# Optimization experiments

Measured on AMD Instinct MI355X. Metric: run time of the kernel, lower is better.

## Reference

```python
import jax, jax.numpy as jnp
import numpy as np


def setup_inputs() -> dict:
    key = jax.random.key(0)
    ks = jax.random.split(key, 15)
    B, r, d, h, na = 64, 64, 2048, 64, 256
    x = jax.random.normal(ks[0], (B, d, na), dtype=jnp.float32)
    L = jax.random.randint(ks[1], (B, 2, na), 0, 2).astype(jnp.float32)
    p = lambda i, shp: jax.random.normal(ks[i], shp, dtype=jnp.float32)
    return {
        "x": x, "L": L,
        "Aq": p(2, (r, d)), "Ak": p(3, (r, d)), "Av": p(4, (r, d)),
        "Aq1": p(5, (r, r)), "Ak1": p(6, (r, r)), "Av1": p(7, (r, r)),
        "Aq5": p(8, (r, r)), "Ak5": p(9, (r, r)), "Av5": p(10, (r, r)),
        "Ao": p(11, (r, r)), "Ao1": p(12, (r, r)), "Ao5": p(13, (h, r)),
    }


def reference(x, L, Aq, Ak, Av, Aq1, Ak1, Av1, Aq5, Ak5, Av5, Ao, Ao1, Ao5):
    B, d, na = x.shape
    # numNeighbors: count of L[:,0,:] >= 1 per batch, +1 -> [B,1,1]
    numN = jnp.sum((L[:, 0, :] >= 1.0).astype(jnp.float32), axis=1)[:, None, None] + 1.0
    scale = jnp.sqrt(numN)  # [B,1,1]

    def attn(M, Wq, Wk, Wv):
        # M: [B, f, na]; Wq/Wk/Wv: [r, f]
        Q = jax.nn.sigmoid(jnp.einsum('rf,bfn->bnr', Wq, M))  # [B,na,r]
        K = jax.nn.sigmoid(jnp.einsum('rf,bfn->brn', Wk, M))  # [B,r,na]
        V = jax.nn.sigmoid(jnp.einsum('rf,bfn->bnr', Wv, M))  # [B,na,r]
        A = jax.nn.softmax(jnp.einsum('bnr,brm->bnm', Q, K) / scale, axis=2)
        return jnp.einsum('bnm,bmr->brn', A, V)  # [B,r,na]

    o = attn(x, Aq, Ak, Av)
    M = jax.nn.silu(jnp.einsum('sr,brn->bsn', Ao, o))
    o = attn(M, Aq1, Ak1, Av1)
    M = jax.nn.silu(jnp.einsum('sr,brn->bsn', Ao1, o))
    o = attn(M, Aq5, Ak5, Av5)
    M = jax.nn.silu(jnp.einsum('hr,brn->bhn', Ao5, o))  # [B,h,na]

    blk = d // na  # rows per block (8)
    def diagvec(i):
        # kron(sum-of-squares, ones(1,2)) == repeat each element twice -> [B, 2*na]
        return jnp.repeat(jnp.sum(M[:, i * blk:(i + 1) * blk, :] ** 2, axis=1), 2, axis=1)

    M11, M12, M21, M22 = diagvec(0), diagvec(1), diagvec(2), diagvec(3)
    Mpp = jnp.sum(M[:, 4 * blk:, :] ** 2, axis=1)  # [B, na]

    # q = x[:, :4, :].transpose(1,2).reshape(B, 4*na) (agent-major ordering)
    q = jnp.transpose(x[:, :4, :], (0, 2, 1)).reshape(B, 4 * na)
    q1, q2 = q[:, :2 * na], q[:, 2 * na:]
    # Block matrix [[diag(M11), diag(M12)], [diag(M21), diag(M22)]] quadratic form,
    # computed without materializing the [B, 4na, 4na] matrix.
    quad = jnp.sum(M11 * q1 * q1 + M12 * q1 * q2 + M21 * q2 * q1 + M22 * q2 * q2,
                   axis=1, keepdims=True)
    return quad + jnp.sum(Mpp, axis=1, keepdims=True)  # [B, 1]
```

## Files before the change

### kernel.cpp

```cpp
#include <hip/hip_runtime.h>
#include <stdint.h>

typedef _Float16 f16;
typedef f16 f16x8 __attribute__((ext_vector_type(8)));
typedef float f32x4 __attribute__((ext_vector_type(4)));

#define MFMA(a,b,c) __builtin_amdgcn_mfma_f32_16x16x32_f16(a, b, c, 0, 0, 0)

__device__ __forceinline__ float sigmoidf_(float z) {
  return __builtin_amdgcn_rcpf(1.0f + __expf(-z));
}

__global__ void prep_kernel(const float* __restrict__ L,
    const float* __restrict__ Aq, const float* __restrict__ Ak, const float* __restrict__ Av,
    const float* __restrict__ Aq1, const float* __restrict__ Ak1, const float* __restrict__ Av1,
    const float* __restrict__ Aq5, const float* __restrict__ Ak5, const float* __restrict__ Av5,
    const float* __restrict__ Ao, const float* __restrict__ Ao1, const float* __restrict__ Ao5,
    float* __restrict__ scale, f16* __restrict__ Wcat, f16* __restrict__ Wsm,
    float* __restrict__ out)
{
  __shared__ float r4[4];
  int blk = blockIdx.x, t = threadIdx.x;
  if (blk < 64) {
    float v = (L[blk * 512 + t] >= 1.0f) ? 1.0f : 0.0f;
    #pragma unroll
    for (int off = 32; off; off >>= 1) v += __shfl_down(v, off);
    if ((t & 63) == 0) r4[t >> 6] = v;
    __syncthreads();
    if (t == 0) scale[blk] = sqrtf(r4[0] + r4[1] + r4[2] + r4[3] + 1.0f);
  } else if (blk < 160) {
    int base = (blk - 64) * 4096;
    for (int i = 0; i < 16; i++) {
      int idx = base + t + i * 256;
      int row = idx >> 11, col = idx & 2047;
      float v = (row < 64) ? Aq[row * 2048 + col]
              : (row < 128) ? Ak[(row - 64) * 2048 + col]
              : Av[(row - 128) * 2048 + col];
      Wcat[idx] = (f16)v;
    }
  } else if (blk < 169) {
    int j = blk - 160;
    const float* s = (j == 0) ? Aq1 : (j == 1) ? Ak1 : (j == 2) ? Av1 : (j == 3) ? Aq5
                   : (j == 4) ? Ak5 : (j == 5) ? Av5 : (j == 6) ? Ao : (j == 7) ? Ao1 : Ao5;
    for (int i = 0; i < 16; i++) { int idx = t + i * 256; Wsm[j * 4096 + idx] = (f16)s[idx]; }
  } else {
    if (t < 64) out[t] = 0.0f;
  }
}

__global__ __launch_bounds__(256) void qkv1_kernel(const float* __restrict__ x,
    const f16* __restrict__ Wcat, f16* __restrict__ Qt, f16* __restrict__ Kt,
    f16* __restrict__ Vg)
{
  int b = blockIdx.y, n0 = blockIdx.x * 32;
  int t = threadIdx.x, lane = t & 63, w = t >> 6;
  int l15 = lane & 15, q = lane >> 4;
  __shared__ f16 xt[2][32 * 72];
  __shared__ f16 wt[2][192 * 72];
  f32x4 acc[2][3] = {};
  const float* xb = x + (size_t)b * 524288 + n0;
  int tn = t & 31, fg = t >> 5;

  int r0 = t >> 3,           c0 = t & 7;
  int r1 = (t + 256) >> 3,   c1 = (t + 256) & 7;
  int r2 = (t + 512) >> 3,   c2 = (t + 512) & 7;
  int r3 = (t + 768) >> 3,   c3 = (t + 768) & 7;
  int r4 = (t + 1024) >> 3,  c4 = (t + 1024) & 7;
  int r5 = (t + 1280) >> 3,  c5 = (t + 1280) & 7;
  const f16* pw0 = Wcat + (size_t)r0 * 2048 + c0 * 8;
  const f16* pw1 = Wcat + (size_t)r1 * 2048 + c1 * 8;
  const f16* pw2 = Wcat + (size_t)r2 * 2048 + c2 * 8;
  const f16* pw3 = Wcat + (size_t)r3 * 2048 + c3 * 8;
  const f16* pw4 = Wcat + (size_t)r4 * 2048 + c4 * 8;
  const f16* pw5 = Wcat + (size_t)r5 * 2048 + c5 * 8;
  const float* px = xb + (size_t)(fg * 8) * 256 + tn;

  float xa0, xa1, xa2, xa3, xa4, xa5, xa6, xa7;
  uint4 wr0, wr1, wr2, wr3, wr4, wr5;

#define LOAD_X(f0n) do {                                                        \
    const float* xp_ = px + (size_t)(f0n) * 256;                                \
    xa0 = xp_[0];    xa1 = xp_[256];  xa2 = xp_[512];  xa3 = xp_[768];          \
    xa4 = xp_[1024]; xa5 = xp_[1280]; xa6 = xp_[1536]; xa7 = xp_[1792];         \
  } while (0)

#define LOAD_W(f0n) do {                                                        \
    wr0 = *(const uint4*)(pw0 + (f0n)); wr1 = *(const uint4*)(pw1 + (f0n));     \
    wr2 = *(const uint4*)(pw2 + (f0n)); wr3 = *(const uint4*)(pw3 + (f0n));     \
    wr4 = *(const uint4*)(pw4 + (f0n)); wr5 = *(const uint4*)(pw5 + (f0n));     \
  } while (0)

#define WRITE_XW(buf) do {                                                      \
    f16x8 pk_;                                                                  \
    pk_[0] = (f16)xa0; pk_[1] = (f16)xa1; pk_[2] = (f16)xa2; pk_[3] = (f16)xa3; \
    pk_[4] = (f16)xa4; pk_[5] = (f16)xa5; pk_[6] = (f16)xa6; pk_[7] = (f16)xa7; \
    *(f16x8*)&xt[buf][tn * 72 + fg * 8] = pk_;                                  \
    f16* wb_ = &wt[buf][0];                                                     \
    *(uint4*)&wb_[r0 * 72 + c0 * 8] = wr0;                                      \
    *(uint4*)&wb_[r1 * 72 + c1 * 8] = wr1;                                      \
    *(uint4*)&wb_[r2 * 72 + c2 * 8] = wr2;                                      \
    *(uint4*)&wb_[r3 * 72 + c3 * 8] = wr3;                                      \
    *(uint4*)&wb_[r4 * 72 + c4 * 8] = wr4;                                      \
    *(uint4*)&wb_[r5 * 72 + c5 * 8] = wr5;                                      \
  } while (0)

  LOAD_X(0);
  LOAD_W(0);
  WRITE_XW(0);
  __syncthreads();

  int cur = 0;
  for (int f0 = 0; f0 < 2048; f0 += 64) {
    int nxt = cur ^ 1;
    bool more = (f0 + 64 < 2048);
    if (more) { LOAD_X(f0 + 64); LOAD_W(f0 + 64); }

    #pragma unroll
    for (int ks = 0; ks < 2; ks++) {
      int k0 = ks * 32 + q * 8;
      f16x8 af[2], bf[3];
      af[0] = *(const f16x8*)&xt[cur][l15 * 72 + k0];
      af[1] = *(const f16x8*)&xt[cur][(16 + l15) * 72 + k0];
      #pragma unroll
      for (int j = 0; j < 3; j++) bf[j] = *(const f16x8*)&wt[cur][((w * 3 + j) * 16 + l15) * 72 + k0];
      #pragma unroll
      for (int nt = 0; nt < 2; nt++)
        #pragma unroll
        for (int j = 0; j < 3; j++)
          acc[nt][j] = MFMA(af[nt], bf[j], acc[nt][j]);
    }

    if (more) WRITE_XW(nxt);
    __syncthreads();
    cur = nxt;
  }
#undef LOAD_X
#undef LOAD_W
#undef WRITE_XW

  #pragma unroll
  for (int nt = 0; nt < 2; nt++)
    #pragma unroll
    for (int j = 0; j < 3; j++) {
      int rr = (w * 3 + j) * 16 + l15;
      float s[4];
      #pragma unroll
      for (int reg = 0; reg < 4; reg++) s[reg] = sigmoidf_(acc[nt][j][reg]);
      int nbase = n0 + nt * 16 + q * 4;
      if (rr < 64) {
        #pragma unroll
        for (int reg = 0; reg < 4; reg++)
          Qt[(size_t)b * 16384 + (size_t)(nbase + reg) * 64 + rr] = (f16)s[reg];
      } else if (rr < 128) {
        #pragma unroll
        for (int reg = 0; reg < 4; reg++)
          Kt[(size_t)b * 16384 + (size_t)(nbase + reg) * 64 + (rr - 64)] = (f16)s[reg];
      } else {
        union { f16 h[4]; uint2 u; } pk;
        #pragma unroll
        for (int reg = 0; reg < 4; reg++) pk.h[reg] = (f16)s[reg];
        *(uint2*)(Vg + (size_t)b * 16384 + (size_t)(rr - 128) * 256 + nbase) = pk.u;
      }
    }
}

template<int LAYER>
__global__ __launch_bounds__(512) void attnB_kernel(const float* __restrict__ x,
    const float* __restrict__ scale, const f16* __restrict__ Wsm,
    const f16* __restrict__ Qtg, const f16* __restrict__ Ktg, const f16* __restrict__ Vgg,
    const f16* __restrict__ Min, f16* __restrict__ Mout, float* __restrict__ out)
{
  int g = blockIdx.x, b = blockIdx.y, n0 = g * 64;
  int t = threadIdx.x, lane = t & 63, w = t >> 6;
  int l15 = lane & 15, q = lane >> 4;
  __shared__ f16 KT[256 * 72];
  __shared__ f16 SM[256 * 72];
  __shared__ f16 VM[64 * 264];
  __shared__ f16 QT[64 * 72];
  __shared__ f16 OT[64 * 72];
  __shared__ float denomS[64];

  float sinv = __builtin_amdgcn_rcpf(scale[b]);
  if (t < 64) denomS[t] = 0.0f;

  if (LAYER == 0) {
    const uint4* qs = (const uint4*)(Qtg + (size_t)b * 16384 + (size_t)n0 * 64);
    { int n = t >> 3, c = t & 7; *(uint4*)&QT[n * 72 + c * 8] = qs[t]; }
    const uint4* ks = (const uint4*)(Ktg + (size_t)b * 16384);
    const uint4* vs = (const uint4*)(Vgg + (size_t)b * 16384);
    #pragma unroll
    for (int i = 0; i < 4; i++) {
      int id = t + i * 512;
      int m = id >> 3, c = id & 7;
      *(uint4*)&KT[m * 72 + c * 8] = ks[id];
      int r = id >> 5, c2 = id & 31;
      *(uint4*)&VM[r * 264 + c2 * 8] = vs[id];
    }
  } else {
    const uint4* ms = (const uint4*)(Min + (size_t)b * 16384);
    #pragma unroll
    for (int i = 0; i < 4; i++) {
      int id = t + i * 512, m = id >> 3, c = id & 7;
      *(uint4*)&SM[m * 72 + c * 8] = ms[id];
    }
  }
  __syncthreads();

  const f16* Wq = Wsm + (size_t)(LAYER == 1 ? 0 : 3) * 4096;
  const f16* Wk = Wsm + (size_t)(LAYER == 1 ? 1 : 4) * 4096;
  const f16* Wv = Wsm + (size_t)(LAYER == 1 ? 2 : 5) * 4096;
  const f16* Wo = Wsm + (size_t)(LAYER == 0 ? 6 : (LAYER == 1 ? 7 : 8)) * 4096;

  if (LAYER > 0) {
    if (w < 4) {
      f16x8 bk[4][2];
      #pragma unroll
      for (int rt = 0; rt < 4; rt++) {
        bk[rt][0] = *(const f16x8*)(Wk + (rt * 16 + l15) * 64 + q * 8);
        bk[rt][1] = *(const f16x8*)(Wk + (rt * 16 + l15) * 64 + 32 + q * 8);
      }
      #pragma unroll
      for (int mi = 0; mi < 4; mi++) {
        int mt = w * 4 + mi;
        f16x8 a0 = *(const f16x8*)&SM[(mt * 16 + l15) * 72 + q * 8];
        f16x8 a1 = *(const f16x8*)&SM[(mt * 16 + l15) * 72 + 32 + q * 8];
        #pragma unroll
        for (int rt = 0; rt < 4; rt++) {
          f32x4 acc = {}; acc = MFMA(a0, bk[rt][0], acc); acc = MFMA(a1, bk[rt][1], acc);
          #pragma unroll
          for (int reg = 0; reg < 4; reg++)
            KT[(mt * 16 + q * 4 + reg) * 72 + rt * 16 + l15] = (f16)sigmoidf_(acc[reg]);
        }
      }
    } else {
      f16x8 av[4][2];
      #pragma unroll
      for (int rt = 0; rt < 4; rt++) {
        av[rt][0] = *(const f16x8*)(Wv + (rt * 16 + l15) * 64 + q * 8);
        av[rt][1] = *(const f16x8*)(Wv + (rt * 16 + l15) * 64 + 32 + q * 8);
      }
      #pragma unroll
      for (int mi = 0; mi < 4; mi++) {
        int mt = (w - 4) * 4 + mi;
        f16x8 b0 = *(const f16x8*)&SM[(mt * 16 + l15) * 72 + q * 8];
        f16x8 b1 = *(const f16x8*)&SM[(mt * 16 + l15) * 72 + 32 + q * 8];
        #pragma unroll
        for (int rt = 0; rt < 4; rt++) {
          f32x4 acc = {}; acc = MFMA(av[rt][0], b0, acc); acc = MFMA(av[rt][1], b1, acc);
          #pragma unroll
          for (int reg = 0; reg < 4; reg++)
            VM[(rt * 16 + q * 4 + reg) * 264 + mt * 16 + l15] = (f16)sigmoidf_(acc[reg]);
        }
      }
    }
    {
      int nt = w >> 1;
      f16x8 a0 = *(const f16x8*)&SM[(n0 + nt * 16 + l15) * 72 + q * 8];
      f16x8 a1 = *(const f16x8*)&SM[(n0 + nt * 16 + l15) * 72 + 32 + q * 8];
      #pragma unroll
      for (int j = 0; j < 2; j++) {
        int rt = (w & 1) * 2 + j;
        f16x8 b0 = *(const f16x8*)(Wq + (rt * 16 + l15) * 64 + q * 8);
        f16x8 b1 = *(const f16x8*)(Wq + (rt * 16 + l15) * 64 + 32 + q * 8);
        f32x4 acc = {}; acc = MFMA(a0, b0, acc); acc = MFMA(a1, b1, acc);
        #pragma unroll
        for (int reg = 0; reg < 4; reg++)
          QT[(nt * 16 + q * 4 + reg) * 72 + rt * 16 + l15] = (f16)sigmoidf_(acc[reg]);
      }
    }
    __syncthreads();
  }

  {
    int nt = w >> 1;
    f16x8 a0 = *(const f16x8*)&QT[(nt * 16 + l15) * 72 + q * 8];
    f16x8 a1 = *(const f16x8*)&QT[(nt * 16 + l15) * 72 + 32 + q * 8];
    float dsum[4] = {0.f, 0.f, 0.f, 0.f};
    #pragma unroll
    for (int mi = 0; mi < 8; mi++) {
      int mt = (w & 1) * 8 + mi;
      f16x8 b0 = *(const f16x8*)&KT[(mt * 16 + l15) * 72 + q * 8];
      f16x8 b1 = *(const f16x8*)&KT[(mt * 16 + l15) * 72 + 32 + q * 8];
      f32x4 acc = {}; acc = MFMA(a0, b0, acc); acc = MFMA(a1, b1, acc);
      #pragma unroll
      for (int reg = 0; reg < 4; reg++) {
        float e = __expf(acc[reg] * sinv);
        dsum[reg] += e;
        SM[(nt * 16 + q * 4 + reg) * 264 + mt * 16 + l15] = (f16)e;
      }
    }
    #pragma unroll
    for (int reg = 0; reg < 4; reg++) {
      #pragma unroll
      for (int mask = 1; mask < 16; mask <<= 1) dsum[reg] += __shfl_xor(dsum[reg], mask);
    }
    if (l15 == 0) {
      #pragma unroll
      for (int reg = 0; reg < 4; reg++) atomicAdd(&denomS[nt * 16 + q * 4 + reg], dsum[reg]);
    }
  }
  __syncthreads();

  {
    int nt = w >> 1;
    f32x4 oacc[2] = {};
    #pragma unroll
    for (int kc = 0; kc < 8; kc++) {
      f16x8 af = *(const f16x8*)&SM[(nt * 16 + l15) * 264 + kc * 32 + q * 8];
      #pragma unroll
      for (int j = 0; j < 2; j++) {
        int rt = (w & 1) * 2 + j;
        f16x8 bf = *(const f16x8*)&VM[(rt * 16 + l15) * 264 + kc * 32 + q * 8];
        oacc[j] = MFMA(af, bf, oacc[j]);
      }
    }
    float rden[4];
    #pragma unroll
    for (int reg = 0; reg < 4; reg++)
      rden[reg] = __builtin_amdgcn_rcpf(denomS[nt * 16 + q * 4 + reg]);
    #pragma unroll
    for (int j = 0; j < 2; j++) {
      int rt = (w & 1) * 2 + j;
      #pragma unroll
      for (int reg = 0; reg < 4; reg++) {
        int row = nt * 16 + q * 4 + reg;
        OT[row * 72 + rt * 16 + l15] = (f16)(oacc[j][reg] * rden[reg]);
      }
    }
  }
  __syncthreads();

  f16* Mst = QT;
  {
    int nt = w >> 1;
    f16x8 a0 = *(const f16x8*)&OT[(nt * 16 + l15) * 72 + q * 8];
    f16x8 a1 = *(const f16x8*)&OT[(nt * 16 + l15) * 72 + 32 + q * 8];
    #pragma unroll
    for (int j = 0; j < 2; j++) {
      int st = (w & 1) * 2 + j;
      f16x8 b0 = *(const f16x8*)(Wo + (st * 16 + l15) * 64 + q * 8);
      f16x8 b1 = *(const f16x8*)(Wo + (st * 16 + l15) * 64 + 32 + q * 8);
      f32x4 acc = {}; acc = MFMA(a0, b0, acc); acc = MFMA(a1, b1, acc);
      #pragma unroll
      for (int reg = 0; reg < 4; reg++) {
        float z = acc[reg];
        Mst[(nt * 16 + q * 4 + reg) * 64 + st * 16 + l15] = (f16)(z * sigmoidf_(z));
      }
    }
  }
  __syncthreads();

  if (LAYER < 2) {
    int row = t >> 3, c = t & 7;
    *(uint4*)(Mout + (size_t)b * 16384 + (size_t)(n0 + row) * 64 + c * 8)
        = *(const uint4*)&Mst[row * 64 + c * 8];
  } else {
    float contrib = 0.0f;
    if (t < 64) {
      int ntok = n0 + t;
      const f16* row = &Mst[t * 64];
      float d[4] = {0, 0, 0, 0}, pp = 0.0f;
      #pragma unroll
      for (int gg = 0; gg < 8; gg++) {
        f16x8 v = *(const f16x8*)(row + gg * 8);
        float ss = 0.0f;
        #pragma unroll
        for (int k = 0; k < 8; k++) { float f = (float)v[k]; ss += f * f; }
        if (gg < 4) d[gg] = ss; else pp += ss;
      }
      int np = ntok >> 1, c0 = (ntok & 1) * 2;
      const float* xb = x + (size_t)b * 524288 + (size_t)c0 * 256;
      float q1a = xb[np], q1b = xb[256 + np];
      float q2a = xb[128 + np], q2b = xb[384 + np];
      contrib = d[0] * (q1a * q1a + q1b * q1b)
              + (d[1] + d[2]) * (q1a * q2a + q1b * q2b)
              + d[3] * (q2a * q2a + q2b * q2b) + pp;
    }
    if (w == 0) {
      #pragma unroll
      for (int off = 32; off; off >>= 1) contrib += __shfl_down(contrib, off);
      if (lane == 0) atomicAdd(out + b, contrib);
    }
  }
}

extern "C" void kernel_launch(void* const* d_in, const int* in_sizes, int n_in,
                              void* d_out, int out_size, void* d_ws, size_t ws_size,
                              hipStream_t stream) {
  const float* x   = (const float*)d_in[0];
  const float* L   = (const float*)d_in[1];
  const float* Aq  = (const float*)d_in[2];
  const float* Ak  = (const float*)d_in[3];
  const float* Av  = (const float*)d_in[4];
  const float* Aq1 = (const float*)d_in[5];
  const float* Ak1 = (const float*)d_in[6];
  const float* Av1 = (const float*)d_in[7];
  const float* Aq5 = (const float*)d_in[8];
  const float* Ak5 = (const float*)d_in[9];
  const float* Av5 = (const float*)d_in[10];
  const float* Ao  = (const float*)d_in[11];
  const float* Ao1 = (const float*)d_in[12];
  const float* Ao5 = (const float*)d_in[13];

  char* ws = (char*)d_ws;
  float* scale = (float*)ws;
  f16* Wcat  = (f16*)(ws + 256);
  f16* Wsm   = (f16*)(ws + 786688);
  f16* Qtg   = (f16*)(ws + 860416);
  f16* Ktg   = (f16*)(ws + 2957568);
  f16* Vgg   = (f16*)(ws + 5054720);
  f16* MbufA = (f16*)(ws + 7151872);
  f16* MbufB = (f16*)(ws + 9249024);
  float* out = (float*)d_out;

  prep_kernel<<<170, 256, 0, stream>>>(L, Aq, Ak, Av, Aq1, Ak1, Av1,
                                       Aq5, Ak5, Av5, Ao, Ao1, Ao5, scale, Wcat, Wsm, out);
  qkv1_kernel<<<dim3(8, 64), 256, 0, stream>>>(x, Wcat, Qtg, Ktg, Vgg);
  attnB_kernel<0><<<dim3(4, 64), 512, 0, stream>>>(x, scale, Wsm, Qtg, Ktg, Vgg,
                                                   nullptr, MbufA, out);
  attnB_kernel<1><<<dim3(4, 64), 512, 0, stream>>>(x, scale, Wsm, Qtg, Ktg, Vgg,
                                                   MbufA, MbufB, out);
  attnB_kernel<2><<<dim3(4, 64), 512, 0, stream>>>(x, scale, Wsm, Qtg, Ktg, Vgg,
                                                   MbufB, nullptr, out);
}
```

Before: 265.4 us.

## Widen qkv1 token tile to 64 and double attention block threads

The QKV projection kernel now uses 512-thread blocks that each cover 64 tokens, so every weight tile staged in shared memory is reused across twice as many tokens and the weight traffic per token is halved. The attention kernels move to 1024 threads per block, giving each wave a smaller slice of the QK, PV and output-projection MFMA work. This is meant to raise parallelism and weight reuse. The cost is half as many qkv1 blocks (256 instead of 512) and heavier block-wide synchronisation, with more idle threads in the copy phases.

```diff
diff --git a/kernel.cpp b/kernel.cpp
--- a/kernel.cpp
+++ b/kernel.cpp
@@ -48,35 +48,30 @@
   }
 }
 
-__global__ __launch_bounds__(256) void qkv1_kernel(const float* __restrict__ x,
+__global__ __launch_bounds__(512, 4) void qkv1_kernel(const float* __restrict__ x,
     const f16* __restrict__ Wcat, f16* __restrict__ Qt, f16* __restrict__ Kt,
     f16* __restrict__ Vg)
 {
-  int b = blockIdx.y, n0 = blockIdx.x * 32;
+  int b = blockIdx.y, n0 = blockIdx.x * 64;
   int t = threadIdx.x, lane = t & 63, w = t >> 6;
   int l15 = lane & 15, q = lane >> 4;
-  __shared__ f16 xt[2][32 * 72];
+  __shared__ f16 xt[2][64 * 72];
   __shared__ f16 wt[2][192 * 72];
   f32x4 acc[2][3] = {};
   const float* xb = x + (size_t)b * 524288 + n0;
-  int tn = t & 31, fg = t >> 5;
+  int tn = t & 63, fg = t >> 6;
+  int nh = w >> 2, wr_ = w & 3;
 
   int r0 = t >> 3,           c0 = t & 7;
-  int r1 = (t + 256) >> 3,   c1 = (t + 256) & 7;
-  int r2 = (t + 512) >> 3,   c2 = (t + 512) & 7;
-  int r3 = (t + 768) >> 3,   c3 = (t + 768) & 7;
-  int r4 = (t + 1024) >> 3,  c4 = (t + 1024) & 7;
-  int r5 = (t + 1280) >> 3,  c5 = (t + 1280) & 7;
+  int r1 = (t + 512) >> 3,   c1 = (t + 512) & 7;
+  int r2 = (t + 1024) >> 3,  c2 = (t + 1024) & 7;
   const f16* pw0 = Wcat + (size_t)r0 * 2048 + c0 * 8;
   const f16* pw1 = Wcat + (size_t)r1 * 2048 + c1 * 8;
   const f16* pw2 = Wcat + (size_t)r2 * 2048 + c2 * 8;
-  const f16* pw3 = Wcat + (size_t)r3 * 2048 + c3 * 8;
-  const f16* pw4 = Wcat + (size_t)r4 * 2048 + c4 * 8;
-  const f16* pw5 = Wcat + (size_t)r5 * 2048 + c5 * 8;
   const float* px = xb + (size_t)(fg * 8) * 256 + tn;
 
   float xa0, xa1, xa2, xa3, xa4, xa5, xa6, xa7;
-  uint4 wr0, wr1, wr2, wr3, wr4, wr5;
+  uint4 wr0, wr1, wr2;
 
 #define LOAD_X(f0n) do {                                                        \
     const float* xp_ = px + (size_t)(f0n) * 256;                                \
@@ -86,8 +81,7 @@
 
 #define LOAD_W(f0n) do {                                                        \
     wr0 = *(const uint4*)(pw0 + (f0n)); wr1 = *(const uint4*)(pw1 + (f0n));     \
-    wr2 = *(const uint4*)(pw2 + (f0n)); wr3 = *(const uint4*)(pw3 + (f0n));     \
-    wr4 = *(const uint4*)(pw4 + (f0n)); wr5 = *(const uint4*)(pw5 + (f0n));     \
+    wr2 = *(const uint4*)(pw2 + (f0n));                                         \
   } while (0)
 
 #define WRITE_XW(buf) do {                                                      \
@@ -99,9 +93,6 @@
     *(uint4*)&wb_[r0 * 72 + c0 * 8] = wr0;                                      \
     *(uint4*)&wb_[r1 * 72 + c1 * 8] = wr1;                                      \
     *(uint4*)&wb_[r2 * 72 + c2 * 8] = wr2;                                      \
-    *(uint4*)&wb_[r3 * 72 + c3 * 8] = wr3;                                      \
-    *(uint4*)&wb_[r4 * 72 + c4 * 8] = wr4;                                      \
-    *(uint4*)&wb_[r5 * 72 + c5 * 8] = wr5;                                      \
   } while (0)
 
   LOAD_X(0);
@@ -119,10 +110,11 @@
     for (int ks = 0; ks < 2; ks++) {
       int k0 = ks * 32 + q * 8;
       f16x8 af[2], bf[3];
-      af[0] = *(const f16x8*)&xt[cur][l15 * 72 + k0];
-      af[1] = *(const f16x8*)&xt[cur][(16 + l15) * 72 + k0];
-      #pragma unroll
-      for (int j = 0; j < 3; j++) bf[j] = *(const f16x8*)&wt[cur][((w * 3 + j) * 16 + l15) * 72 + k0];
+      af[0] = *(const f16x8*)&xt[cur][(nh * 32 + l15) * 72 + k0];
+      af[1] = *(const f16x8*)&xt[cur][(nh * 32 + 16 + l15) * 72 + k0];
+      #pragma unroll
+      for (int j = 0; j < 3; j++)
+        bf[j] = *(const f16x8*)&wt[cur][((wr_ * 3 + j) * 16 + l15) * 72 + k0];
       #pragma unroll
       for (int nt = 0; nt < 2; nt++)
         #pragma unroll
@@ -142,11 +134,11 @@
   for (int nt = 0; nt < 2; nt++)
     #pragma unroll
     for (int j = 0; j < 3; j++) {
-      int rr = (w * 3 + j) * 16 + l15;
+      int rr = (wr_ * 3 + j) * 16 + l15;
       float s[4];
       #pragma unroll
       for (int reg = 0; reg < 4; reg++) s[reg] = sigmoidf_(acc[nt][j][reg]);
-      int nbase = n0 + nt * 16 + q * 4;
+      int nbase = n0 + nh * 32 + nt * 16 + q * 4;
       if (rr < 64) {
         #pragma unroll
         for (int reg = 0; reg < 4; reg++)
@@ -165,7 +157,7 @@
 }
 
 template<int LAYER>
-__global__ __launch_bounds__(512) void attnB_kernel(const float* __restrict__ x,
+__global__ __launch_bounds__(1024) void attnB_kernel(const float* __restrict__ x,
     const float* __restrict__ scale, const f16* __restrict__ Wsm,
     const f16* __restrict__ Qtg, const f16* __restrict__ Ktg, const f16* __restrict__ Vgg,
     const f16* __restrict__ Min, f16* __restrict__ Mout, float* __restrict__ out)
@@ -184,13 +176,15 @@
   if (t < 64) denomS[t] = 0.0f;
 
   if (LAYER == 0) {
-    const uint4* qs = (const uint4*)(Qtg + (size_t)b * 16384 + (size_t)n0 * 64);
-    { int n = t >> 3, c = t & 7; *(uint4*)&QT[n * 72 + c * 8] = qs[t]; }
+    if (t < 512) {
+      const uint4* qs = (const uint4*)(Qtg + (size_t)b * 16384 + (size_t)n0 * 64);
+      int n = t >> 3, c = t & 7; *(uint4*)&QT[n * 72 + c * 8] = qs[t];
+    }
     const uint4* ks = (const uint4*)(Ktg + (size_t)b * 16384);
     const uint4* vs = (const uint4*)(Vgg + (size_t)b * 16384);
     #pragma unroll
-    for (int i = 0; i < 4; i++) {
-      int id = t + i * 512;
+    for (int i = 0; i < 2; i++) {
+      int id = t + i * 1024;
       int m = id >> 3, c = id & 7;
       *(uint4*)&KT[m * 72 + c * 8] = ks[id];
       int r = id >> 5, c2 = id & 31;
@@ -199,8 +193,8 @@
   } else {
     const uint4* ms = (const uint4*)(Min + (size_t)b * 16384);
     #pragma unroll
-    for (int i = 0; i < 4; i++) {
-      int id = t + i * 512, m = id >> 3, c = id & 7;
+    for (int i = 0; i < 2; i++) {
+      int id = t + i * 1024, m = id >> 3, c = id & 7;
       *(uint4*)&SM[m * 72 + c * 8] = ms[id];
     }
   }
@@ -212,7 +206,7 @@
   const f16* Wo = Wsm + (size_t)(LAYER == 0 ? 6 : (LAYER == 1 ? 7 : 8)) * 4096;
 
   if (LAYER > 0) {
-    if (w < 4) {
+    if (w < 8) {
       f16x8 bk[4][2];
       #pragma unroll
       for (int rt = 0; rt < 4; rt++) {
@@ -220,8 +214,8 @@
         bk[rt][1] = *(const f16x8*)(Wk + (rt * 16 + l15) * 64 + 32 + q * 8);
       }
       #pragma unroll
-      for (int mi = 0; mi < 4; mi++) {
-        int mt = w * 4 + mi;
+      for (int mi = 0; mi < 2; mi++) {
+        int mt = w * 2 + mi;
         f16x8 a0 = *(const f16x8*)&SM[(mt * 16 + l15) * 72 + q * 8];
         f16x8 a1 = *(const f16x8*)&SM[(mt * 16 + l15) * 72 + 32 + q * 8];
         #pragma unroll
@@ -240,8 +234,8 @@
         av[rt][1] = *(const f16x8*)(Wv + (rt * 16 + l15) * 64 + 32 + q * 8);
       }
       #pragma unroll
-      for (int mi = 0; mi < 4; mi++) {
-        int mt = (w - 4) * 4 + mi;
+      for (int mi = 0; mi < 2; mi++) {
+        int mt = (w - 8) * 2 + mi;
         f16x8 b0 = *(const f16x8*)&SM[(mt * 16 + l15) * 72 + q * 8];
         f16x8 b1 = *(const f16x8*)&SM[(mt * 16 + l15) * 72 + 32 + q * 8];
         #pragma unroll
@@ -254,31 +248,27 @@
       }
     }
     {
-      int nt = w >> 1;
+      int nt = w >> 2, rt = w & 3;
       f16x8 a0 = *(const f16x8*)&SM[(n0 + nt * 16 + l15) * 72 + q * 8];
       f16x8 a1 = *(const f16x8*)&SM[(n0 + nt * 16 + l15) * 72 + 32 + q * 8];
-      #pragma unroll
-      for (int j = 0; j < 2; j++) {
-        int rt = (w & 1) * 2 + j;
-        f16x8 b0 = *(const f16x8*)(Wq + (rt * 16 + l15) * 64 + q * 8);
-        f16x8 b1 = *(const f16x8*)(Wq + (rt * 16 + l15) * 64 + 32 + q * 8);
-        f32x4 acc = {}; acc = MFMA(a0, b0, acc); acc = MFMA(a1, b1, acc);
-        #pragma unroll
-        for (int reg = 0; reg < 4; reg++)
-          QT[(nt * 16 + q * 4 + reg) * 72 + rt * 16 + l15] = (f16)sigmoidf_(acc[reg]);
-      }
+      f16x8 b0 = *(const f16x8*)(Wq + (rt * 16 + l15) * 64 + q * 8);
+      f16x8 b1 = *(const f16x8*)(Wq + (rt * 16 + l15) * 64 + 32 + q * 8);
+      f32x4 acc = {}; acc = MFMA(a0, b0, acc); acc = MFMA(a1, b1, acc);
+      #pragma unroll
+      for (int reg = 0; reg < 4; reg++)
+        QT[(nt * 16 + q * 4 + reg) * 72 + rt * 16 + l15] = (f16)sigmoidf_(acc[reg]);
     }
     __syncthreads();
   }
 
   {
-    int nt = w >> 1;
+    int nt = w >> 2;
     f16x8 a0 = *(const f16x8*)&QT[(nt * 16 + l15) * 72 + q * 8];
     f16x8 a1 = *(const f16x8*)&QT[(nt * 16 + l15) * 72 + 32 + q * 8];
     float dsum[4] = {0.f, 0.f, 0.f, 0.f};
     #pragma unroll
-    for (int mi = 0; mi < 8; mi++) {
-      int mt = (w & 1) * 8 + mi;
+    for (int mi = 0; mi < 4; mi++) {
+      int mt = (w & 3) * 4 + mi;
       f16x8 b0 = *(const f16x8*)&KT[(mt * 16 + l15) * 72 + q * 8];
       f16x8 b1 = *(const f16x8*)&KT[(mt * 16 + l15) * 72 + 32 + q * 8];
       f32x4 acc = {}; acc = MFMA(a0, b0, acc); acc = MFMA(a1, b1, acc);
@@ -302,58 +292,48 @@
   __syncthreads();
 
   {
-    int nt = w >> 1;
-    f32x4 oacc[2] = {};
+    int nt = w >> 2, rt = w & 3;
+    f32x4 oacc = {};
     #pragma unroll
     for (int kc = 0; kc < 8; kc++) {
       f16x8 af = *(const f16x8*)&SM[(nt * 16 + l15) * 264 + kc * 32 + q * 8];
-      #pragma unroll
-      for (int j = 0; j < 2; j++) {
-        int rt = (w & 1) * 2 + j;
-        f16x8 bf = *(const f16x8*)&VM[(rt * 16 + l15) * 264 + kc * 32 + q * 8];
-        oacc[j] = MFMA(af, bf, oacc[j]);
-      }
+      f16x8 bf = *(const f16x8*)&VM[(rt * 16 + l15) * 264 + kc * 32 + q * 8];
+      oacc = MFMA(af, bf, oacc);
     }
     float rden[4];
     #pragma unroll
     for (int reg = 0; reg < 4; reg++)
       rden[reg] = __builtin_amdgcn_rcpf(denomS[nt * 16 + q * 4 + reg]);
     #pragma unroll
-    for (int j = 0; j < 2; j++) {
-      int rt = (w & 1) * 2 + j;
-      #pragma unroll
-      for (int reg = 0; reg < 4; reg++) {
-        int row = nt * 16 + q * 4 + reg;
-        OT[row * 72 + rt * 16 + l15] = (f16)(oacc[j][reg] * rden[reg]);
-      }
+    for (int reg = 0; reg < 4; reg++) {
+      int row = nt * 16 + q * 4 + reg;
+      OT[row * 72 + rt * 16 + l15] = (f16)(oacc[reg] * rden[reg]);
     }
   }
   __syncthreads();
 
   f16* Mst = QT;
   {
-    int nt = w >> 1;
+    int nt = w >> 2, st = w & 3;
     f16x8 a0 = *(const f16x8*)&OT[(nt * 16 + l15) * 72 + q * 8];
     f16x8 a1 = *(const f16x8*)&OT[(nt * 16 + l15) * 72 + 32 + q * 8];
-    #pragma unroll
-    for (int j = 0; j < 2; j++) {
-      int st = (w & 1) * 2 + j;
-      f16x8 b0 = *(const f16x8*)(Wo + (st * 16 + l15) * 64 + q * 8);
-      f16x8 b1 = *(const f16x8*)(Wo + (st * 16 + l15) * 64 + 32 + q * 8);
-      f32x4 acc = {}; acc = MFMA(a0, b0, acc); acc = MFMA(a1, b1, acc);
-      #pragma unroll
-      for (int reg = 0; reg < 4; reg++) {
-        float z = acc[reg];
-        Mst[(nt * 16 + q * 4 + reg) * 64 + st * 16 + l15] = (f16)(z * sigmoidf_(z));
-      }
+    f16x8 b0 = *(const f16x8*)(Wo + (st * 16 + l15) * 64 + q * 8);
+    f16x8 b1 = *(const f16x8*)(Wo + (st * 16 + l15) * 64 + 32 + q * 8);
+    f32x4 acc = {}; acc = MFMA(a0, b0, acc); acc = MFMA(a1, b1, acc);
+    #pragma unroll
+    for (int reg = 0; reg < 4; reg++) {
+      float z = acc[reg];
+      Mst[(nt * 16 + q * 4 + reg) * 64 + st * 16 + l15] = (f16)(z * sigmoidf_(z));
     }
   }
   __syncthreads();
 
   if (LAYER < 2) {
-    int row = t >> 3, c = t & 7;
-    *(uint4*)(Mout + (size_t)b * 16384 + (size_t)(n0 + row) * 64 + c * 8)
-        = *(const uint4*)&Mst[row * 64 + c * 8];
+    if (t < 512) {
+      int row = t >> 3, c = t & 7;
+      *(uint4*)(Mout + (size_t)b * 16384 + (size_t)(n0 + row) * 64 + c * 8)
+          = *(const uint4*)&Mst[row * 64 + c * 8];
+    }
   } else {
     float contrib = 0.0f;
     if (t < 64) {
@@ -415,11 +395,11 @@
 
   prep_kernel<<<170, 256, 0, stream>>>(L, Aq, Ak, Av, Aq1, Ak1, Av1,
                                        Aq5, Ak5, Av5, Ao, Ao1, Ao5, scale, Wcat, Wsm, out);
-  qkv1_kernel<<<dim3(8, 64), 256, 0, stream>>>(x, Wcat, Qtg, Ktg, Vgg);
-  attnB_kernel<0><<<dim3(4, 64), 512, 0, stream>>>(x, scale, Wsm, Qtg, Ktg, Vgg,
-                                                   nullptr, MbufA, out);
-  attnB_kernel<1><<<dim3(4, 64), 512, 0, stream>>>(x, scale, Wsm, Qtg, Ktg, Vgg,
-                                                   MbufA, MbufB, out);
-  attnB_kernel<2><<<dim3(4, 64), 512, 0, stream>>>(x, scale, Wsm, Qtg, Ktg, Vgg,
-                                                   MbufB, nullptr, out);
+  qkv1_kernel<<<dim3(4, 64), 512, 0, stream>>>(x, Wcat, Qtg, Ktg, Vgg);
+  attnB_kernel<0><<<dim3(4, 64), 1024, 0, stream>>>(x, scale, Wsm, Qtg, Ktg, Vgg,
+                                                    nullptr, MbufA, out);
+  attnB_kernel<1><<<dim3(4, 64), 1024, 0, stream>>>(x, scale, Wsm, Qtg, Ktg, Vgg,
+                                                    MbufA, MbufB, out);
+  attnB_kernel<2><<<dim3(4, 64), 1024, 0, stream>>>(x, scale, Wsm, Qtg, Ktg, Vgg,
+                                                    MbufB, nullptr, out);
 }
```

New measurement: 265.6 us. No clear change (+0.1%).
